# Optimization experiments

Measured on AMD Instinct MI355X. Metric: run time of the kernel, lower is better.

## Reference

```python
import jax, jax.numpy as jnp
import numpy as np


def _cdist(x, y):
    # Euclidean (p=2) pairwise distances, matching torch.cdist.
    # x: [B, N, D], y: [B, M, D] -> [B, N, M]
    xx = jnp.sum(x * x, axis=-1)                      # [B, N]
    yy = jnp.sum(y * y, axis=-1)                      # [B, M]
    zz = jnp.einsum('bnd,bmd->bnm', x, y)             # [B, N, M]
    d2 = xx[:, :, None] + yy[:, None, :] - 2.0 * zz
    return jnp.sqrt(jnp.maximum(d2, 0.0))


def setup_inputs() -> dict:
    key = jax.random.key(0)
    k1, k2 = jax.random.split(key)
    gts = jax.random.normal(k1, (4, 8192, 3), dtype=jnp.float32)
    preds = jax.random.normal(k2, (4, 8192, 3), dtype=jnp.float32)
    return {"gts": gts, "preds": preds}


def reference(gts, preds):
    P = _cdist(gts, preds)                 # [B, N, M]
    loss_1 = jnp.sum(jnp.min(P, axis=1), axis=1)  # min over gts points, sum over preds
    loss_2 = jnp.sum(jnp.min(P, axis=2), axis=1)  # min over preds points, sum over gts
    return loss_1 + loss_2                 # [B]
```

## Files before the change

### kernel.cpp

```cpp
#include <hip/hip_runtime.h>
#include <math.h>

#define BB 4
#define NPTS 8192
#define THREADS 512
#define NQ_TOTAL (2 * BB * NPTS)
#define QBLK 512
#define QPWV 64
#define QUARTN 2048
#define CHUNK 2048
#define NFRAG (CHUNK / 32)
#define GLDS_PER_WAVE (CHUNK / 8 / 64)
#define FBLK 512

typedef __attribute__((ext_vector_type(8)))  short bf16x8;
typedef __attribute__((ext_vector_type(16))) float f32x16;


__device__ __forceinline__ unsigned short f2bf(float f) {
    unsigned u = __float_as_uint(f);
    u += 0x7FFF + ((u >> 16) & 1);
    return (unsigned short)(u >> 16);
}
__device__ __forceinline__ float bf2f(unsigned short h) {
    return __uint_as_float(((unsigned)h) << 16);
}

__global__ __launch_bounds__(256) void pack_kernel(
    const float* __restrict__ gts, const float* __restrict__ preds,
    uint4* __restrict__ refpack, uint4* __restrict__ qpack,
    unsigned* __restrict__ minpart, float* __restrict__ out) {
    int idx = blockIdx.x * 256 + threadIdx.x;
    if (idx < BB) out[idx] = 0.0f;
    if (idx >= NQ_TOTAL) return;
    minpart[idx] = 0x7F7FFFFFu;
    int set  = idx / (BB * NPTS);
    int pidx = idx - set * (BB * NPTS);
    const float* src = set ? preds : gts;
    unsigned short hx = f2bf(src[pidx * 3 + 0]);
    unsigned short hy = f2bf(src[pidx * 3 + 1]);
    unsigned short hz = f2bf(src[pidx * 3 + 2]);
    float fx = bf2f(hx), fy = bf2f(hy), fz = bf2f(hz);
    float rr = fmaf(fx, fx, fmaf(fy, fy, fz * fz));
    unsigned short hrr = f2bf(rr);
    unsigned short hlo = f2bf(rr - bf2f(hrr));
    const unsigned short ONE = 0x3F80;

    uint4 rv;
    rv.x = (unsigned)hx  | ((unsigned)hy  << 16);
    rv.y = (unsigned)hz  | ((unsigned)hrr << 16);
    rv.z = (unsigned)hlo | ((unsigned)ONE << 16);
    rv.w = (unsigned)ONE;
    refpack[idx] = rv;

    unsigned short nx = f2bf(-2.0f * fx);
    unsigned short ny = f2bf(-2.0f * fy);
    unsigned short nz = f2bf(-2.0f * fz);
    uint4 qv;
    qv.x = (unsigned)nx  | ((unsigned)ny  << 16);
    qv.y = (unsigned)nz  | ((unsigned)ONE << 16);
    qv.z = (unsigned)ONE | ((unsigned)hrr << 16);
    qv.w = (unsigned)hlo;
    qpack[idx] = qv;
}

#define FOLD8(P, X0, X1, X2, X3)                                   \
    X0 = fminf(fminf((P)[0],  (P)[1]),  X0);                       \
    X1 = fminf(fminf((P)[2],  (P)[3]),  X1);                       \
    X2 = fminf(fminf((P)[4],  (P)[5]),  X2);                       \
    X3 = fminf(fminf((P)[6],  (P)[7]),  X3);                       \
    X0 = fminf(fminf((P)[8],  (P)[9]),  X0);                       \
    X1 = fminf(fminf((P)[10], (P)[11]), X1);                       \
    X2 = fminf(fminf((P)[12], (P)[13]), X2);                       \
    X3 = fminf(fminf((P)[14], (P)[15]), X3);

#define STEP(AQ, FN, DO_LOAD)                                               \
    {                                                                       \
        f32x16 d0 = __builtin_amdgcn_mfma_f32_32x32x16_bf16(AQ, bq0, zc, 0, 0, 0); \
        f32x16 d1 = __builtin_amdgcn_mfma_f32_32x32x16_bf16(AQ, bq1, zc, 0, 0, 0); \
        if (DO_LOAD) AQ = sp[(FN) * 32 + l31];                              \
        FOLD8(d0, c0, c1, c2, c3);                                          \
        FOLD8(d1, c4, c5, c6, c7);                                          \
    }

#define STAGE()                                                             \
    _Pragma("unroll")                                                       \
    for (int i = 0; i < GLDS_PER_WAVE; ++i)                                 \
        __builtin_amdgcn_global_load_lds(                                   \
            (const unsigned*)(rgl + wid * 256 + i * 64 + lane),             \
            (unsigned*)&sref[wid * 256 + i * 64], 16, 0, 0);

__global__ __launch_bounds__(THREADS, 4) void chamfer_kernel(
    const uint4* __restrict__ refpack, const uint4* __restrict__ qpack,
    unsigned* __restrict__ minpart) {
    __shared__ uint4 sref[CHUNK];

    int tid  = threadIdx.x;
    int blk  = blockIdx.x;
    int quart= blk >> 7;
    int dir  = (blk >> 6) & 1;
    int b    = (blk >> 4) & 3;
    int qg   = blk & 15;
    int rset = dir;
    int qset = dir ^ 1;
    int wid  = tid >> 6;
    int lane = tid & 63;
    int l31  = lane & 31;

    const uint4* rgl = refpack + (size_t)(rset * BB + b) * NPTS
                     + (size_t)quart * QUARTN;

    STAGE();

    size_t qoff = (size_t)(qset * BB + b) * NPTS + (size_t)qg * QBLK
                + (size_t)wid * QPWV;
    bf16x8 bq0 = {0, 0, 0, 0, 0, 0, 0, 0};
    bf16x8 bq1 = {0, 0, 0, 0, 0, 0, 0, 0};
    if (lane < 32) {
        bq0 = ((const bf16x8*)qpack)[qoff + l31];
        bq1 = ((const bf16x8*)qpack)[qoff + 32 + l31];
    }
    __syncthreads();

    f32x16 zc;
    #pragma unroll
    for (int r = 0; r < 16; ++r) zc[r] = 0.0f;

    float c0 = 3.0e38f, c1 = 3.0e38f, c2 = 3.0e38f, c3 = 3.0e38f;
    float c4 = 3.0e38f, c5 = 3.0e38f, c6 = 3.0e38f, c7 = 3.0e38f;

    const bf16x8* sp = (const bf16x8*)sref;

    bf16x8 a0 = sp[0 * 32 + l31];
    bf16x8 a1 = sp[1 * 32 + l31];
    bf16x8 a2 = sp[2 * 32 + l31];
    bf16x8 a3 = sp[3 * 32 + l31];

    #pragma unroll
    for (int m = 0; m < NFRAG / 4; ++m) {
        const bool L = (m < NFRAG / 4 - 1);
        STEP(a0, (m + 1) * 4 + 0, L);
        STEP(a1, (m + 1) * 4 + 1, L);
        STEP(a2, (m + 1) * 4 + 2, L);
        STEP(a3, (m + 1) * 4 + 3, L);
    }

    float m0 = fminf(fminf(c0, c1), fminf(c2, c3));
    m0 = fminf(m0, __shfl_xor(m0, 32, 64));
    float m1 = fminf(fminf(c4, c5), fminf(c6, c7));
    m1 = fminf(m1, __shfl_xor(m1, 32, 64));

    size_t qid = (size_t)(dir * BB + b) * NPTS + (size_t)qg * QBLK
               + (size_t)wid * QPWV;
    if (lane < 32) {
        atomicMin(minpart + qid + l31,      __float_as_uint(fmaxf(m0, 0.0f)));
        atomicMin(minpart + qid + 32 + l31, __float_as_uint(fmaxf(m1, 0.0f)));
    }
}

__global__ __launch_bounds__(256) void merge_kernel(
    const unsigned* __restrict__ minpart, float* __restrict__ out) {
    int t  = blockIdx.x * 256 + threadIdx.x;
    uint4 v = ((const uint4*)minpart)[t];
    float d = sqrtf(__uint_as_float(v.x)) + sqrtf(__uint_as_float(v.y))
            + sqrtf(__uint_as_float(v.z)) + sqrtf(__uint_as_float(v.w));
    int b = (blockIdx.x >> 3) & 3;

    #pragma unroll
    for (int off = 32; off > 0; off >>= 1)
        d += __shfl_down(d, off, 64);

    __shared__ float wsum[4];
    int lane = threadIdx.x & 63;
    int wid  = threadIdx.x >> 6;
    if (lane == 0) wsum[wid] = d;
    __syncthreads();
    if (threadIdx.x == 0)
        atomicAdd(out + b, wsum[0] + wsum[1] + wsum[2] + wsum[3]);
}

extern "C" void kernel_launch(void* const* d_in, const int* in_sizes, int n_in,
                              void* d_out, int out_size, void* d_ws, size_t ws_size,
                              hipStream_t stream) {
    const float* gts   = (const float*)d_in[0];
    const float* preds = (const float*)d_in[1];
    float* out = (float*)d_out;

    char* ws = (char*)d_ws;
    uint4*    refpack = (uint4*)ws;
    uint4*    qpack   = (uint4*)(ws + (size_t)NQ_TOTAL * 16);
    unsigned* minpart = (unsigned*)(ws + (size_t)NQ_TOTAL * 32);

    pack_kernel<<<NQ_TOTAL / 256, 256, 0, stream>>>(
        gts, preds, refpack, qpack, minpart, out);

    chamfer_kernel<<<FBLK, THREADS, 0, stream>>>(refpack, qpack, minpart);

    merge_kernel<<<NQ_TOTAL / 4 / 256, 256, 0, stream>>>(minpart, out);
}
```

Baseline: 72.44 us.

## Switch distance MFMA to 32x32x8 bf16 with K split into two planes

Replaces the 32x32x16 bf16 MFMA, whose K of 16 was half zero padding, with the 32x32x8 bf16_1k variant. To match it, the packed 8-element rows are split into two 4-element planes (lo and hi). The two 32-lane halves of a wave each supply one plane, so no lanes hold padding. The aim is cheaper matrix instructions per distance tile. In exchange the pack and staging layout changes, and correctness depends on the 1k variant's lane-to-K mapping matching this split.

```diff
diff --git a/kernel.cpp b/kernel.cpp
--- a/kernel.cpp
+++ b/kernel.cpp
@@ -8,12 +8,10 @@
 #define QBLK 512
 #define QPWV 64
 #define QUARTN 2048
-#define CHUNK 2048
-#define NFRAG (CHUNK / 32)
-#define GLDS_PER_WAVE (CHUNK / 8 / 64)
+#define NFRAG (QUARTN / 32)
 #define FBLK 512
 
-typedef __attribute__((ext_vector_type(8)))  short bf16x8;
+typedef __attribute__((ext_vector_type(4)))  short bf16x4;
 typedef __attribute__((ext_vector_type(16))) float f32x16;
 
 
@@ -28,7 +26,7 @@
 
 __global__ __launch_bounds__(256) void pack_kernel(
     const float* __restrict__ gts, const float* __restrict__ preds,
-    uint4* __restrict__ refpack, uint4* __restrict__ qpack,
+    uint2* __restrict__ refpl, uint2* __restrict__ qpl,
     unsigned* __restrict__ minpart, float* __restrict__ out) {
     int idx = blockIdx.x * 256 + threadIdx.x;
     if (idx < BB) out[idx] = 0.0f;
@@ -46,22 +44,24 @@
     unsigned short hlo = f2bf(rr - bf2f(hrr));
     const unsigned short ONE = 0x3F80;
 
-    uint4 rv;
-    rv.x = (unsigned)hx  | ((unsigned)hy  << 16);
-    rv.y = (unsigned)hz  | ((unsigned)hrr << 16);
-    rv.z = (unsigned)hlo | ((unsigned)ONE << 16);
-    rv.w = (unsigned)ONE;
-    refpack[idx] = rv;
+    uint2 rlo, rhi;
+    rlo.x = (unsigned)hx  | ((unsigned)hy  << 16);
+    rlo.y = (unsigned)hz  | ((unsigned)hrr << 16);
+    rhi.x = (unsigned)hlo | ((unsigned)ONE << 16);
+    rhi.y = (unsigned)ONE;
+    refpl[idx]            = rlo;
+    refpl[NQ_TOTAL + idx] = rhi;
 
     unsigned short nx = f2bf(-2.0f * fx);
     unsigned short ny = f2bf(-2.0f * fy);
     unsigned short nz = f2bf(-2.0f * fz);
-    uint4 qv;
-    qv.x = (unsigned)nx  | ((unsigned)ny  << 16);
-    qv.y = (unsigned)nz  | ((unsigned)ONE << 16);
-    qv.z = (unsigned)ONE | ((unsigned)hrr << 16);
-    qv.w = (unsigned)hlo;
-    qpack[idx] = qv;
+    uint2 qlo, qhi;
+    qlo.x = (unsigned)nx  | ((unsigned)ny  << 16);
+    qlo.y = (unsigned)nz  | ((unsigned)ONE << 16);
+    qhi.x = (unsigned)ONE | ((unsigned)hrr << 16);
+    qhi.y = (unsigned)hlo;
+    qpl[idx]            = qlo;
+    qpl[NQ_TOTAL + idx] = qhi;
 }
 
 #define FOLD8(P, X0, X1, X2, X3)                                   \
@@ -74,26 +74,32 @@
     X2 = fminf(fminf((P)[12], (P)[13]), X2);                       \
     X3 = fminf(fminf((P)[14], (P)[15]), X3);
 
+#define MFMA8(A, B, C) __builtin_amdgcn_mfma_f32_32x32x8bf16_1k(A, B, C, 0, 0, 0)
+
 #define STEP(AQ, FN, DO_LOAD)                                               \
     {                                                                       \
-        f32x16 d0 = __builtin_amdgcn_mfma_f32_32x32x16_bf16(AQ, bq0, zc, 0, 0, 0); \
-        f32x16 d1 = __builtin_amdgcn_mfma_f32_32x32x16_bf16(AQ, bq1, zc, 0, 0, 0); \
-        if (DO_LOAD) AQ = sp[(FN) * 32 + l31];                              \
+        f32x16 d0 = MFMA8(AQ, bq0, zc);                                     \
+        f32x16 d1 = MFMA8(AQ, bq1, zc);                                     \
+        if (DO_LOAD) AQ = spv[poff + (FN) * 32 + l31];                      \
         FOLD8(d0, c0, c1, c2, c3);                                          \
         FOLD8(d1, c4, c5, c6, c7);                                          \
     }
 
 #define STAGE()                                                             \
     _Pragma("unroll")                                                       \
-    for (int i = 0; i < GLDS_PER_WAVE; ++i)                                 \
+    for (int i = 0; i < 2; ++i) {                                           \
         __builtin_amdgcn_global_load_lds(                                   \
-            (const unsigned*)(rgl + wid * 256 + i * 64 + lane),             \
-            (unsigned*)&sref[wid * 256 + i * 64], 16, 0, 0);
+            (const unsigned*)(rlo_src + i * 1024 + wid * 128 + lane * 2),   \
+            (unsigned*)&sref[0][i * 1024 + wid * 128], 16, 0, 0);           \
+        __builtin_amdgcn_global_load_lds(                                   \
+            (const unsigned*)(rhi_src + i * 1024 + wid * 128 + lane * 2),   \
+            (unsigned*)&sref[1][i * 1024 + wid * 128], 16, 0, 0);           \
+    }
 
 __global__ __launch_bounds__(THREADS, 4) void chamfer_kernel(
-    const uint4* __restrict__ refpack, const uint4* __restrict__ qpack,
+    const uint2* __restrict__ refpl, const uint2* __restrict__ qpl,
     unsigned* __restrict__ minpart) {
-    __shared__ uint4 sref[CHUNK];
+    __shared__ uint2 sref[2][QUARTN];
 
     int tid  = threadIdx.x;
     int blk  = blockIdx.x;
@@ -106,20 +112,19 @@
     int wid  = tid >> 6;
     int lane = tid & 63;
     int l31  = lane & 31;
-
-    const uint4* rgl = refpack + (size_t)(rset * BB + b) * NPTS
-                     + (size_t)quart * QUARTN;
+    int khalf= lane >> 5;
+
+    size_t rbase = (size_t)(rset * BB + b) * NPTS + (size_t)quart * QUARTN;
+    const uint2* rlo_src = refpl + rbase;
+    const uint2* rhi_src = refpl + NQ_TOTAL + rbase;
 
     STAGE();
 
     size_t qoff = (size_t)(qset * BB + b) * NPTS + (size_t)qg * QBLK
                 + (size_t)wid * QPWV;
-    bf16x8 bq0 = {0, 0, 0, 0, 0, 0, 0, 0};
-    bf16x8 bq1 = {0, 0, 0, 0, 0, 0, 0, 0};
-    if (lane < 32) {
-        bq0 = ((const bf16x8*)qpack)[qoff + l31];
-        bq1 = ((const bf16x8*)qpack)[qoff + 32 + l31];
-    }
+    const bf16x4* qv = (const bf16x4*)qpl;
+    bf16x4 bq0 = qv[(size_t)khalf * NQ_TOTAL + qoff + l31];
+    bf16x4 bq1 = qv[(size_t)khalf * NQ_TOTAL + qoff + 32 + l31];
     __syncthreads();
 
     f32x16 zc;
@@ -129,12 +134,13 @@
     float c0 = 3.0e38f, c1 = 3.0e38f, c2 = 3.0e38f, c3 = 3.0e38f;
     float c4 = 3.0e38f, c5 = 3.0e38f, c6 = 3.0e38f, c7 = 3.0e38f;
 
-    const bf16x8* sp = (const bf16x8*)sref;
-
-    bf16x8 a0 = sp[0 * 32 + l31];
-    bf16x8 a1 = sp[1 * 32 + l31];
-    bf16x8 a2 = sp[2 * 32 + l31];
-    bf16x8 a3 = sp[3 * 32 + l31];
+    const bf16x4* spv = (const bf16x4*)sref;
+    const int poff = khalf * QUARTN;
+
+    bf16x4 a0 = spv[poff + 0 * 32 + l31];
+    bf16x4 a1 = spv[poff + 1 * 32 + l31];
+    bf16x4 a2 = spv[poff + 2 * 32 + l31];
+    bf16x4 a3 = spv[poff + 3 * 32 + l31];
 
     #pragma unroll
     for (int m = 0; m < NFRAG / 4; ++m) {
@@ -187,14 +193,14 @@
     float* out = (float*)d_out;
 
     char* ws = (char*)d_ws;
-    uint4*    refpack = (uint4*)ws;
-    uint4*    qpack   = (uint4*)(ws + (size_t)NQ_TOTAL * 16);
+    uint2*    refpl   = (uint2*)ws;
+    uint2*    qpl     = (uint2*)(ws + (size_t)NQ_TOTAL * 16);
     unsigned* minpart = (unsigned*)(ws + (size_t)NQ_TOTAL * 32);
 
     pack_kernel<<<NQ_TOTAL / 256, 256, 0, stream>>>(
-        gts, preds, refpack, qpack, minpart, out);
-
-    chamfer_kernel<<<FBLK, THREADS, 0, stream>>>(refpack, qpack, minpart);
+        gts, preds, refpl, qpl, minpart, out);
+
+    chamfer_kernel<<<FBLK, THREADS, 0, stream>>>(refpl, qpl, minpart);
 
     merge_kernel<<<NQ_TOTAL / 4 / 256, 256, 0, stream>>>(minpart, out);
 }
```

New measurement: 71.47 us. No clear change (-1.3%).
